# Optimization experiments

Hardware: AMD Instinct MI355X
Metric: run time of the kernel (lower is better)

Reference implementation:

```python
import jax, jax.numpy as jnp
import numpy as np
import math

B, S, E, H = 2, 2048, 1024, 16
D = E // H
EPS = 1e-5


def setup_inputs() -> dict:
    key = jax.random.key(0)
    ks = jax.random.split(key, 6)
    s = 1.0 / math.sqrt(E)
    return {
        "query": jax.random.normal(ks[0], (B, S, E), jnp.float32),
        "Wq": jax.random.normal(ks[1], (E, E), jnp.float32) * s,
        "bq": jnp.zeros((E,), jnp.float32),
        "Wk": jax.random.normal(ks[2], (E, E), jnp.float32) * s,
        "bk": jnp.zeros((E,), jnp.float32),
        "Wv": jax.random.normal(ks[3], (E, E), jnp.float32) * s,
        "bv": jnp.zeros((E,), jnp.float32),
        "Wo": jax.random.normal(ks[4], (E, E), jnp.float32) * s,
        "bo": jnp.zeros((E,), jnp.float32),
        "alpha": jnp.ones((1,), jnp.float32),
    }


def reference(query, Wq, bq, Wk, bk, Wv, bv, Wo, bo, alpha):
    # Q/K/V projections (nn.Linear: x @ W.T + b)
    q = (query @ Wq.T + bq).reshape(B, S, H, D)
    k = (query @ Wk.T + bk).reshape(B, S, H, D)
    v = (query @ Wv.T + bv).reshape(B, S, H, D)

    # YAT scores: (q.k)^2 / (||q-k||^2 + eps)
    qk = jnp.einsum('bqhd,bkhd->bhqk', q, k)          # [B,H,S,S]
    sq = jnp.einsum('bqhd,bqhd->bhq', q, q)           # ||q||^2
    sk = jnp.einsum('bkhd,bkhd->bhk', k, k)           # ||k||^2
    dist_sq = sq[..., :, None] + sk[..., None, :] - 2.0 * qk
    scores = (qk * qk) / (dist_sq + EPS)

    # learnable alpha scaling: scores * (sqrt(d)/log(1+d))^alpha
    scale = (jnp.sqrt(jnp.float32(D)) / jnp.log1p(jnp.float32(D))) ** alpha[0]
    scores = scores * scale

    attn = jax.nn.softmax(scores, axis=-1)
    out = jnp.einsum('bhqk,bkhd->bqhd', attn, v).reshape(B, S, E)
    return out @ Wo.T + bo
```

## Files before the change

kernel.cpp:

```cpp
#include <hip/hip_runtime.h>
#include <hip/hip_fp16.h>
#include <math.h>

#define BB 2
#define SS 2048
#define EE 1024
#define HH 16
#define DD 64
#define YAT_EPS 1e-5f
#define RR (BB * HH * SS)

typedef __attribute__((ext_vector_type(8))) short bf16x8;
typedef __attribute__((ext_vector_type(4))) short short4v;
typedef __attribute__((ext_vector_type(4))) float f32x4;
#define MFMA16(a, b, c) __builtin_amdgcn_mfma_f32_16x16x32_bf16((a), (b), (c), 0, 0, 0)

#if __has_builtin(__builtin_amdgcn_exp2f)
#define EXP2(x) __builtin_amdgcn_exp2f(x)
#else
#define EXP2(x) exp2f(x)
#endif
#if __has_builtin(__builtin_amdgcn_rcpf)
#define RCPF(x) __builtin_amdgcn_rcpf(x)
#else
#define RCPF(x) (1.0f / (x))
#endif

__device__ __forceinline__ unsigned short f2bf(float x) {
    unsigned int u = __float_as_uint(x);
    u += 0x7FFFu + ((u >> 16) & 1u);
    return (unsigned short)(u >> 16);
}
__device__ __forceinline__ float bf2f(unsigned short h) {
    return __uint_as_float(((unsigned int)h) << 16);
}
__device__ __forceinline__ short f2bf_t(float x) {
    return (short)(__float_as_uint(x) >> 16);
}

__device__ __forceinline__ void async_ld16(void* lds, const void* g) {
    __builtin_amdgcn_global_load_lds(
        (const __attribute__((address_space(1))) unsigned int*)g,
        (__attribute__((address_space(3))) unsigned int*)lds, 16, 0, 0);
}

__global__ __launch_bounds__(256) void split_f32(const float* __restrict__ in,
                                                 unsigned short* __restrict__ hi,
                                                 unsigned short* __restrict__ lo,
                                                 int n4) {
    int i = blockIdx.x * 256 + threadIdx.x;
    if (i >= n4) return;
    float4 v = ((const float4*)in)[i];
    ushort4 h, l;
    h.x = f2bf(v.x); l.x = f2bf(v.x - bf2f(h.x));
    h.y = f2bf(v.y); l.y = f2bf(v.y - bf2f(h.y));
    h.z = f2bf(v.z); l.z = f2bf(v.z - bf2f(h.z));
    h.w = f2bf(v.w); l.w = f2bf(v.w - bf2f(h.w));
    ((ushort4*)hi)[i] = h;
    ((ushort4*)lo)[i] = l;
}

__global__ __launch_bounds__(256) void split_w4(
        const float* __restrict__ Wq, const float* __restrict__ Wk,
        const float* __restrict__ Wv, const float* __restrict__ Wo,
        unsigned short* __restrict__ Whi, unsigned short* __restrict__ Wlo,
        unsigned short* __restrict__ Wohi) {
    int i = blockIdx.x * 256 + threadIdx.x;
    int y = blockIdx.y;
    const float* src = y == 0 ? Wq : y == 1 ? Wk : y == 2 ? Wv : Wo;
    unsigned short* hi = y < 3 ? Whi + (size_t)y * EE * EE : Wohi;
    float4 v = ((const float4*)src)[i];
    ushort4 h;
    h.x = f2bf(v.x); h.y = f2bf(v.y); h.z = f2bf(v.z); h.w = f2bf(v.w);
    ((ushort4*)hi)[i] = h;
    if (y < 2) {
        unsigned short* lo = Wlo + (size_t)y * EE * EE;
        ushort4 l;
        l.x = f2bf(v.x - bf2f(h.x));
        l.y = f2bf(v.y - bf2f(h.y));
        l.z = f2bf(v.z - bf2f(h.z));
        l.w = f2bf(v.w - bf2f(h.w));
        ((ushort4*)lo)[i] = l;
    }
}

template <int MODE, int PASSES>
__global__ __launch_bounds__(256, 2) void gemm3p(
        const unsigned short* __restrict__ Ahi, const unsigned short* __restrict__ Alo,
        const unsigned short* __restrict__ Bhi, const unsigned short* __restrict__ Blo,
        const float* __restrict__ bq, const float* __restrict__ bk,
        const float* __restrict__ bv,
        float* __restrict__ Cf,
        unsigned short* __restrict__ qhi, unsigned short* __restrict__ qlo,
        unsigned short* __restrict__ khi,
        unsigned short* __restrict__ v_sd,
        float* __restrict__ sqn, float* __restrict__ skn,
        int M, int N, int K) {
    __shared__ __align__(16) unsigned short LA_hi[128 * 32];
    __shared__ __align__(16) unsigned short LA_lo[128 * 32];
    __shared__ __align__(16) unsigned short LB_hi[128 * 32];
    __shared__ __align__(16) unsigned short LB_lo[128 * 32];

    const int t = threadIdx.x;
    const int w = t >> 6, lane = t & 63;
    const int quad = lane >> 4, lr = lane & 15;
    const int wy = w & 1, wx = w >> 1;
    const int m0 = blockIdx.y * 128, n0 = blockIdx.x * 128;

    const unsigned short* gsrc = nullptr;
    unsigned short* ldst = nullptr;
    if (w == 0)      { gsrc = Ahi + (size_t)m0 * K; ldst = LA_hi; }
    else if (w == 2) { gsrc = Bhi + (size_t)n0 * K; ldst = LB_hi; }
    else if (PASSES == 3 && w == 1) { gsrc = Alo + (size_t)m0 * K; ldst = LA_lo; }
    else if (PASSES == 3 && w == 3) { gsrc = Blo + (size_t)n0 * K; ldst = LB_lo; }
    const unsigned short* gl = gsrc ? gsrc + (size_t)(lane >> 2) * K + (lane & 3) * 8
                                    : nullptr;

    f32x4 acc[4][4];
    #pragma unroll
    for (int i = 0; i < 4; ++i)
        #pragma unroll
        for (int j = 0; j < 4; ++j)
            acc[i][j] = (f32x4){0.f, 0.f, 0.f, 0.f};

    for (int k0 = 0; k0 < K; k0 += 32) {
        __syncthreads();
        if (gl) {
            #pragma unroll
            for (int i = 0; i < 8; ++i)
                async_ld16(ldst + i * 512, gl + (size_t)i * 16 * K + k0);
        }
        __syncthreads();
        bf16x8 ah[4], al[4], bh_[4], bl_[4];
        #pragma unroll
        for (int i = 0; i < 4; ++i) {
            ah[i]  = *(const bf16x8*)&LA_hi[(wy * 64 + i * 16 + lr) * 32 + quad * 8];
            bh_[i] = *(const bf16x8*)&LB_hi[(wx * 64 + i * 16 + lr) * 32 + quad * 8];
            if (PASSES == 3) {
                al[i]  = *(const bf16x8*)&LA_lo[(wy * 64 + i * 16 + lr) * 32 + quad * 8];
                bl_[i] = *(const bf16x8*)&LB_lo[(wx * 64 + i * 16 + lr) * 32 + quad * 8];
            }
        }
        #pragma unroll
        for (int mg = 0; mg < 4; ++mg)
            #pragma unroll
            for (int ns = 0; ns < 4; ++ns) {
                f32x4 a = acc[mg][ns];
                a = MFMA16(ah[mg], bh_[ns], a);
                if (PASSES == 3) {
                    a = MFMA16(ah[mg], bl_[ns], a);
                    a = MFMA16(al[mg], bh_[ns], a);
                }
                acc[mg][ns] = a;
            }
    }

    const int ng = n0 + wx * 64;
    if (MODE == 0) {
        float bias_v[4];
        #pragma unroll
        for (int ns = 0; ns < 4; ++ns) bias_v[ns] = bq[ng + ns * 16 + lr];
        #pragma unroll
        for (int mg = 0; mg < 4; ++mg)
            #pragma unroll
            for (int r = 0; r < 4; ++r) {
                int m = m0 + wy * 64 + mg * 16 + quad * 4 + r;
                #pragma unroll
                for (int ns = 0; ns < 4; ++ns)
                    Cf[(size_t)m * N + ng + ns * 16 + lr] = acc[mg][ns][r] + bias_v[ns];
            }
    } else {
        const int path = MODE == 1 ? (ng >> 10) : 2;
        const int c = MODE == 1 ? (ng & 1023) : ng;
        const int h = c >> 6;
        const float* bias = path == 0 ? bq : path == 1 ? bk : bv;
        unsigned short* hi_p = path == 0 ? qhi : path == 1 ? khi : v_sd;
        float* nrm = path == 0 ? sqn : skn;
        float bias_v[4];
        #pragma unroll
        for (int ns = 0; ns < 4; ++ns) bias_v[ns] = bias[c + ns * 16 + lr];
        #pragma unroll
        for (int mg = 0; mg < 4; ++mg)
            #pragma unroll
            for (int r = 0; r < 4; ++r) {
                int m = m0 + wy * 64 + mg * 16 + quad * 4 + r;
                int b = m >> 11, s = m & (SS - 1);
                size_t base = ((size_t)(b * HH + h) * SS + s) * DD;
                float v4[4];
                #pragma unroll
                for (int ns = 0; ns < 4; ++ns) v4[ns] = acc[mg][ns][r] + bias_v[ns];
                if (path < 2) {
                    float pn = v4[0] * v4[0] + v4[1] * v4[1] + v4[2] * v4[2] + v4[3] * v4[3];
                    #pragma unroll
                    for (int off = 1; off < 16; off <<= 1) pn += __shfl_xor(pn, off);
                    if (lr == 0) nrm[(size_t)(b * HH + h) * SS + s] = pn;
                    #pragma unroll
                    for (int ns = 0; ns < 4; ++ns) {
                        unsigned short hv = f2bf(v4[ns]);
                        hi_p[base + ns * 16 + lr] = hv;
                        if (path == 0)
                            qlo[base + ns * 16 + lr] = f2bf(v4[ns] - bf2f(hv));
                    }
                } else {
                    #pragma unroll
                    for (int ns = 0; ns < 4; ++ns)
                        hi_p[base + ns * 16 + lr] = f2bf(v4[ns]);
                }
            }
    }
}

__global__ __launch_bounds__(256) void transpose_v(const unsigned short* __restrict__ v_sd,
                                                   unsigned short* __restrict__ vt) {
    __shared__ unsigned short T[64][65];
    const int t = threadIdx.x;
    const int bh = blockIdx.y, s0 = blockIdx.x * 64;
    {
        int sl = t >> 2, d4 = (t & 3) * 16;
        const unsigned short* src = &v_sd[((size_t)bh * SS + s0 + sl) * DD + d4];
        bf16x8 a = *(const bf16x8*)src;
        bf16x8 b = *(const bf16x8*)(src + 8);
        #pragma unroll
        for (int j = 0; j < 8; ++j) {
            T[sl][d4 + j] = (unsigned short)a[j];
            T[sl][d4 + 8 + j] = (unsigned short)b[j];
        }
    }
    __syncthreads();
    {
        int dl = t >> 2, s4 = (t & 3) * 16;
        bf16x8 a, b;
        #pragma unroll
        for (int j = 0; j < 8; ++j) {
            a[j] = (short)T[s4 + j][dl];
            b[j] = (short)T[s4 + 8 + j][dl];
        }
        unsigned short* dst = &vt[((size_t)bh * DD + dl) * SS + s0 + s4];
        *(bf16x8*)dst = a;
        *(bf16x8*)(dst + 8) = b;
    }
}

__global__ __launch_bounds__(256, 4) void yat_attn_mfma(
        const unsigned short* __restrict__ qhi, const unsigned short* __restrict__ qlo,
        const unsigned short* __restrict__ khi,
        const unsigned short* __restrict__ vt,
        const float* __restrict__ sqn, const float* __restrict__ skn,
        const float* __restrict__ alphap,
        __half* __restrict__ Opart, float2* __restrict__ mlpart) {
    __shared__ __align__(16) unsigned short Ks[2][4096];
    __shared__ __align__(16) unsigned short Ps[4][16 * 68];

    const int t = threadIdx.x;
    const int w = t >> 6, lane = t & 63;
    const int quad = lane >> 4, lr = lane & 15;
    const int qt = blockIdx.x, bh = blockIdx.y, z = blockIdx.z;
    const int row0 = qt * 64 + w * 16;
    const float cscale = powf(sqrtf((float)DD) / log1pf((float)DD), alphap[0])
                         * 1.4426950408889634f;

    bf16x8 qh[2], ql[2];
    #pragma unroll
    for (int kd = 0; kd < 2; ++kd) {
        size_t o = ((size_t)bh * SS + row0 + lr) * DD + kd * 32 + quad * 8;
        qh[kd] = *(const bf16x8*)&qhi[o];
        ql[kd] = *(const bf16x8*)&qlo[o];
    }
    const float sqe = sqn[(size_t)bh * SS + row0 + lr] + YAT_EPS;

    const int lrow = lane >> 3;
    const int lofs = lrow * 64 + (((lane & 7) ^ (lrow & 7)) << 3);
    const int sw = lr & 7;

    float m_r = -INFINITY, l_r = 0.f;
    f32x4 O[4];
    #pragma unroll
    for (int nd = 0; nd < 4; ++nd) O[nd] = (f32x4){0.f, 0.f, 0.f, 0.f};

    const int t0 = z * 16;
    const size_t khi_base = (size_t)bh * SS * 64 + (size_t)w * 16 * 64 + lofs;
    const size_t skn_base = (size_t)bh * SS + quad * 4;
    unsigned short* myP = Ps[w];

    #pragma unroll
    for (int i2 = 0; i2 < 2; ++i2)
        async_ld16(&Ks[0][w * 1024 + i2 * 512],
                   khi + khi_base + (size_t)t0 * 4096 + i2 * 512);

    for (int it = 0; it < 16; ++it) {
        const int p = it & 1;
        __syncthreads();
        if (it + 1 < 16) {
            #pragma unroll
            for (int i2 = 0; i2 < 2; ++i2)
                async_ld16(&Ks[p ^ 1][w * 1024 + i2 * 512],
                           khi + khi_base + (size_t)(t0 + it + 1) * 4096 + i2 * 512);
        }
        const int kbase = (t0 + it) * 64;
        const unsigned short* kb = Ks[p];
        f32x4 acc[4];
        f32x4 sk4[4];
        #pragma unroll
        for (int st = 0; st < 4; ++st) {
            const int rbase = (st * 16 + lr) * 64;
            bf16x8 kh0 = *(const bf16x8*)&kb[rbase + ((quad    ) ^ sw) * 8];
            bf16x8 kh1 = *(const bf16x8*)&kb[rbase + ((quad + 4) ^ sw) * 8];
            sk4[st] = *(const f32x4*)&skn[skn_base + kbase + st * 16];
            f32x4 a = (f32x4){0.f, 0.f, 0.f, 0.f};
            a = MFMA16(kh0, qh[0], a);
            a = MFMA16(kh1, qh[1], a);
            a = MFMA16(kh0, ql[0], a);
            a = MFMA16(kh1, ql[1], a);
            acc[st] = a;
        }
        bf16x8 vf[4][2];
        #pragma unroll
        for (int nd = 0; nd < 4; ++nd)
            #pragma unroll
            for (int kk = 0; kk < 2; ++kk)
                vf[nd][kk] = *(const bf16x8*)&vt[((size_t)bh * DD + nd * 16 + lr) * SS
                                                 + kbase + kk * 32 + quad * 8];
        float mx = -INFINITY;
        #pragma unroll
        for (int st = 0; st < 4; ++st)
            #pragma unroll
            for (int r = 0; r < 4; ++r) {
                float qk = acc[st][r];
                float d = sqe + sk4[st][r] - 2.f * qk;
                float u = qk * qk * RCPF(d);
                acc[st][r] = u;
                mx = fmaxf(mx, u);
            }
        mx = fmaxf(mx, __shfl_xor(mx, 16));
        mx = fmaxf(mx, __shfl_xor(mx, 32));
        float mnew = fmaxf(m_r, mx);
        bool resc = !__all(cscale * (mnew - m_r) <= 8.f);
        float aa = 1.f;
        if (resc) {
            aa = EXP2(__builtin_fmaf(cscale, m_r, -cscale * mnew));
            m_r = mnew;
        }
        const float cm = cscale * m_r;
        float rs = 0.f;
        #pragma unroll
        for (int st = 0; st < 4; ++st) {
            float e0 = EXP2(__builtin_fmaf(cscale, acc[st][0], -cm));
            float e1 = EXP2(__builtin_fmaf(cscale, acc[st][1], -cm));
            float e2 = EXP2(__builtin_fmaf(cscale, acc[st][2], -cm));
            float e3 = EXP2(__builtin_fmaf(cscale, acc[st][3], -cm));
            rs += (e0 + e1) + (e2 + e3);
            short4v pv;
            pv[0] = f2bf_t(e0); pv[1] = f2bf_t(e1);
            pv[2] = f2bf_t(e2); pv[3] = f2bf_t(e3);
            *(short4v*)&myP[lr * 68 + st * 16 + quad * 4] = pv;
        }
        rs += __shfl_xor(rs, 16);
        rs += __shfl_xor(rs, 32);
        l_r = l_r * aa + rs;
        if (resc) {
            float al_[4];
            #pragma unroll
            for (int r = 0; r < 4; ++r) al_[r] = __shfl(aa, quad * 4 + r);
            #pragma unroll
            for (int nd = 0; nd < 4; ++nd)
                #pragma unroll
                for (int r = 0; r < 4; ++r)
                    O[nd][r] *= al_[r];
        }
        bf16x8 pf[2];
        #pragma unroll
        for (int kk = 0; kk < 2; ++kk)
            pf[kk] = *(const bf16x8*)&myP[lr * 68 + kk * 32 + quad * 8];
        #pragma unroll
        for (int nd = 0; nd < 4; ++nd)
            #pragma unroll
            for (int kk = 0; kk < 2; ++kk)
                O[nd] = MFMA16(pf[kk], vf[nd][kk], O[nd]);
    }
    if (quad == 0)
        mlpart[(size_t)z * RR + (size_t)bh * SS + row0 + lr] =
            make_float2(cscale * m_r, l_r);
    #pragma unroll
    for (int r = 0; r < 4; ++r) {
        size_t rowg = (size_t)bh * SS + row0 + quad * 4 + r;
        #pragma unroll
        for (int nd = 0; nd < 4; ++nd)
            Opart[((size_t)z * RR + rowg) * DD + nd * 16 + lr] =
                __float2half(O[nd][r]);
    }
}

__global__ __launch_bounds__(256) void combine_attn(
        const __half* __restrict__ Opart, const float2* __restrict__ mlpart,
        unsigned short* __restrict__ ctxhi) {
    int tid = blockIdx.x * 256 + threadIdx.x;
    int row = tid >> 4, c4 = (tid & 15) * 4;
    float2 ml0 = mlpart[row];
    float2 ml1 = mlpart[RR + row];
    float ms = fmaxf(ml0.x, ml1.x);
    float a0 = EXP2(ml0.x - ms), a1 = EXP2(ml1.x - ms);
    float inv = RCPF(ml0.y * a0 + ml1.y * a1);
    a0 *= inv; a1 *= inv;
    const __half* p0 = Opart + (size_t)row * DD + c4;
    const __half* p1 = p0 + (size_t)RR * DD;
    int bh = row >> 11, s = row & (SS - 1);
    int b = bh >> 4, h = bh & 15;
    size_t idx = ((size_t)b * SS + s) * EE + h * DD + c4;
    ushort4 hv;
    unsigned short* hp = (unsigned short*)&hv;
    #pragma unroll
    for (int j = 0; j < 4; ++j) {
        float o = __half2float(p0[j]) * a0 + __half2float(p1[j]) * a1;
        hp[j] = f2bf(o);
    }
    *(ushort4*)&ctxhi[idx] = hv;
}

extern "C" void kernel_launch(void* const* d_in, const int* in_sizes, int n_in,
                              void* d_out, int out_size, void* d_ws, size_t ws_size,
                              hipStream_t stream) {
    const float* x     = (const float*)d_in[0];
    const float* Wq    = (const float*)d_in[1];
    const float* bq    = (const float*)d_in[2];
    const float* Wk    = (const float*)d_in[3];
    const float* bk    = (const float*)d_in[4];
    const float* Wv    = (const float*)d_in[5];
    const float* bv    = (const float*)d_in[6];
    const float* Wo    = (const float*)d_in[7];
    const float* bo    = (const float*)d_in[8];
    const float* alpha = (const float*)d_in[9];
    float* out = (float*)d_out;
    char* ws = (char*)d_ws;

    const int M = BB * SS;
    const size_t MB = 1u << 20;
    unsigned short* xhi  = (unsigned short*)(ws + 0 * MB);
    unsigned short* xlo  = (unsigned short*)(ws + 8 * MB);
    unsigned short* Whi  = (unsigned short*)(ws + 16 * MB);
    unsigned short* Wlo  = (unsigned short*)(ws + 22 * MB);
    unsigned short* vt   = (unsigned short*)(ws + 16 * MB);
    float2* mlpart       = (float2*)(ws + 24 * MB);
    unsigned short* Wohi = (unsigned short*)(ws + 28 * MB);
    unsigned short* qhi  = (unsigned short*)(ws + 32 * MB);
    unsigned short* qlo  = (unsigned short*)(ws + 40 * MB);
    unsigned short* khi  = (unsigned short*)(ws + 48 * MB);
    unsigned short* v_sd = (unsigned short*)(ws + 64 * MB);
    __half* Opart        = (__half*)(ws + 64 * MB);
    float* sqn = (float*)(ws + 80 * MB);
    float* skn = (float*)(ws + 80 * MB + 256 * 1024);
    unsigned short* ctxhi = xhi;

    const int nX = M * EE / 4, nW = EE * EE / 4;
    split_f32<<<nX / 256, 256, 0, stream>>>(x, xhi, xlo, nX);
    split_w4<<<dim3(nW / 256, 4), 256, 0, stream>>>(Wq, Wk, Wv, Wo, Whi, Wlo, Wohi);

    gemm3p<1, 3><<<dim3(2 * EE / 128, M / 128), 256, 0, stream>>>(
        xhi, xlo, Whi, Wlo, bq, bk, nullptr, nullptr,
        qhi, qlo, khi, nullptr, sqn, skn, M, 2 * EE, EE);
    gemm3p<2, 1><<<dim3(EE / 128, M / 128), 256, 0, stream>>>(
        xhi, nullptr, Whi + 2 * (size_t)EE * EE, nullptr, nullptr, nullptr, bv, nullptr,
        nullptr, nullptr, nullptr, v_sd, nullptr, nullptr, M, EE, EE);

    transpose_v<<<dim3(SS / 64, BB * HH), 256, 0, stream>>>(v_sd, vt);

    yat_attn_mfma<<<dim3(SS / 64, BB * HH, 2), 256, 0, stream>>>(
        qhi, qlo, khi, vt, sqn, skn, alpha, Opart, mlpart);

    combine_attn<<<RR * 16 / 256, 256, 0, stream>>>(Opart, mlpart, ctxhi);

    gemm3p<0, 1><<<dim3(EE / 128, M / 128), 256, 0, stream>>>(
        ctxhi, nullptr, Wohi, nullptr, bo, nullptr, nullptr, out,
        nullptr, nullptr, nullptr, nullptr, nullptr, nullptr, M, EE, EE);
}
```

Baseline: 358.2 us.

## Replace shared-memory K staging with register double-buffered direct global loads

Drops the LDS double buffer for K and the per-iteration __syncthreads. Each wave now loads its K fragments straight from global memory into registers, double-buffered across a manually unrolled pair of iterations. It also raises wave priority around the MFMA sections and lowers the occupancy hint from 4 to 3 blocks per CU to leave room for the extra registers. The aim is to remove barrier stalls and LDS traffic, at the cost of more register pressure and redundant global/L2 reads, since every wave now fetches the full K tile itself.

```diff
diff --git a/kernel.cpp b/kernel.cpp
--- a/kernel.cpp
+++ b/kernel.cpp
@@ -241,14 +241,121 @@
     }
 }
 
-__global__ __launch_bounds__(256, 4) void yat_attn_mfma(
+__device__ __forceinline__ void k_load(bf16x8 (&dst)[8],
+                                       const unsigned short* __restrict__ khi,
+                                       size_t krow, int tile, int lr, int quad) {
+    const unsigned short* kp = khi + (krow + (size_t)tile * 64) * DD;
+    dst[0] = *(const bf16x8*)&kp[(0 * 16 + lr) * 64      + quad * 8];
+    dst[1] = *(const bf16x8*)&kp[(0 * 16 + lr) * 64 + 32 + quad * 8];
+    dst[2] = *(const bf16x8*)&kp[(1 * 16 + lr) * 64      + quad * 8];
+    dst[3] = *(const bf16x8*)&kp[(1 * 16 + lr) * 64 + 32 + quad * 8];
+    dst[4] = *(const bf16x8*)&kp[(2 * 16 + lr) * 64      + quad * 8];
+    dst[5] = *(const bf16x8*)&kp[(2 * 16 + lr) * 64 + 32 + quad * 8];
+    dst[6] = *(const bf16x8*)&kp[(3 * 16 + lr) * 64      + quad * 8];
+    dst[7] = *(const bf16x8*)&kp[(3 * 16 + lr) * 64 + 32 + quad * 8];
+}
+
+__device__ __forceinline__ void yat_iter(
+        int itn, int t0,
+        const unsigned short* __restrict__ khi, size_t krow,
+        const unsigned short* __restrict__ vt, size_t vrow,
+        const float* __restrict__ skn, size_t skn_base,
+        const bf16x8 (&kcur)[8], bf16x8 (&knxt)[8],
+        const bf16x8 (&qh)[2], const bf16x8 (&ql)[2],
+        float sqe, float cscale,
+        unsigned short* myP, int lr, int quad,
+        float& m_r, float& l_r, f32x4 (&O)[4]) {
+    const int kbase = (t0 + itn) * 64;
+    if (itn + 1 < 16)
+        k_load(knxt, khi, krow, t0 + itn + 1, lr, quad);
+
+    f32x4 acc[4], sk4[4];
+    __builtin_amdgcn_s_setprio(1);
+    #pragma unroll
+    for (int st = 0; st < 4; ++st) {
+        sk4[st] = *(const f32x4*)&skn[skn_base + kbase + st * 16];
+        f32x4 a = (f32x4){0.f, 0.f, 0.f, 0.f};
+        a = MFMA16(kcur[st * 2], qh[0], a);
+        a = MFMA16(kcur[st * 2 + 1], qh[1], a);
+        a = MFMA16(kcur[st * 2], ql[0], a);
+        a = MFMA16(kcur[st * 2 + 1], ql[1], a);
+        acc[st] = a;
+    }
+    __builtin_amdgcn_s_setprio(0);
+    bf16x8 vf[4][2];
+    #pragma unroll
+    for (int nd = 0; nd < 4; ++nd)
+        #pragma unroll
+        for (int kk = 0; kk < 2; ++kk)
+            vf[nd][kk] = *(const bf16x8*)&vt[(vrow + nd * 16 + lr) * SS
+                                             + kbase + kk * 32 + quad * 8];
+    float mx = -INFINITY;
+    #pragma unroll
+    for (int st = 0; st < 4; ++st)
+        #pragma unroll
+        for (int r = 0; r < 4; ++r) {
+            float qk = acc[st][r];
+            float d = sqe + sk4[st][r] - 2.f * qk;
+            float u = qk * qk * RCPF(d);
+            acc[st][r] = u;
+            mx = fmaxf(mx, u);
+        }
+    mx = fmaxf(mx, __shfl_xor(mx, 16));
+    mx = fmaxf(mx, __shfl_xor(mx, 32));
+    float mnew = fmaxf(m_r, mx);
+    bool resc = !__all(cscale * (mnew - m_r) <= 8.f);
+    float aa = 1.f;
+    if (resc) {
+        aa = EXP2(__builtin_fmaf(cscale, m_r, -cscale * mnew));
+        m_r = mnew;
+    }
+    const float cm = cscale * m_r;
+    float rs = 0.f;
+    #pragma unroll
+    for (int st = 0; st < 4; ++st) {
+        float e0 = EXP2(__builtin_fmaf(cscale, acc[st][0], -cm));
+        float e1 = EXP2(__builtin_fmaf(cscale, acc[st][1], -cm));
+        float e2 = EXP2(__builtin_fmaf(cscale, acc[st][2], -cm));
+        float e3 = EXP2(__builtin_fmaf(cscale, acc[st][3], -cm));
+        rs += (e0 + e1) + (e2 + e3);
+        short4v pv;
+        pv[0] = f2bf_t(e0); pv[1] = f2bf_t(e1);
+        pv[2] = f2bf_t(e2); pv[3] = f2bf_t(e3);
+        *(short4v*)&myP[lr * 68 + st * 16 + quad * 4] = pv;
+    }
+    rs += __shfl_xor(rs, 16);
+    rs += __shfl_xor(rs, 32);
+    l_r = l_r * aa + rs;
+    if (resc) {
+        float al_[4];
+        #pragma unroll
+        for (int r = 0; r < 4; ++r) al_[r] = __shfl(aa, quad * 4 + r);
+        #pragma unroll
+        for (int nd = 0; nd < 4; ++nd)
+            #pragma unroll
+            for (int r = 0; r < 4; ++r)
+                O[nd][r] *= al_[r];
+    }
+    bf16x8 pf[2];
+    #pragma unroll
+    for (int kk = 0; kk < 2; ++kk)
+        pf[kk] = *(const bf16x8*)&myP[lr * 68 + kk * 32 + quad * 8];
+    __builtin_amdgcn_s_setprio(1);
+    #pragma unroll
+    for (int nd = 0; nd < 4; ++nd)
+        #pragma unroll
+        for (int kk = 0; kk < 2; ++kk)
+            O[nd] = MFMA16(pf[kk], vf[nd][kk], O[nd]);
+    __builtin_amdgcn_s_setprio(0);
+}
+
+__global__ __launch_bounds__(256, 3) void yat_attn_mfma(
         const unsigned short* __restrict__ qhi, const unsigned short* __restrict__ qlo,
         const unsigned short* __restrict__ khi,
         const unsigned short* __restrict__ vt,
         const float* __restrict__ sqn, const float* __restrict__ skn,
         const float* __restrict__ alphap,
         __half* __restrict__ Opart, float2* __restrict__ mlpart) {
-    __shared__ __align__(16) unsigned short Ks[2][4096];
     __shared__ __align__(16) unsigned short Ps[4][16 * 68];
 
     const int t = threadIdx.x;
@@ -268,115 +375,27 @@
     }
     const float sqe = sqn[(size_t)bh * SS + row0 + lr] + YAT_EPS;
 
-    const int lrow = lane >> 3;
-    const int lofs = lrow * 64 + (((lane & 7) ^ (lrow & 7)) << 3);
-    const int sw = lr & 7;
-
     float m_r = -INFINITY, l_r = 0.f;
     f32x4 O[4];
     #pragma unroll
     for (int nd = 0; nd < 4; ++nd) O[nd] = (f32x4){0.f, 0.f, 0.f, 0.f};
 
     const int t0 = z * 16;
-    const size_t khi_base = (size_t)bh * SS * 64 + (size_t)w * 16 * 64 + lofs;
+    const size_t krow = (size_t)bh * SS;
+    const size_t vrow = (size_t)bh * DD;
     const size_t skn_base = (size_t)bh * SS + quad * 4;
     unsigned short* myP = Ps[w];
 
-    #pragma unroll
-    for (int i2 = 0; i2 < 2; ++i2)
-        async_ld16(&Ks[0][w * 1024 + i2 * 512],
-                   khi + khi_base + (size_t)t0 * 4096 + i2 * 512);
-
-    for (int it = 0; it < 16; ++it) {
-        const int p = it & 1;
-        __syncthreads();
-        if (it + 1 < 16) {
-            #pragma unroll
-            for (int i2 = 0; i2 < 2; ++i2)
-                async_ld16(&Ks[p ^ 1][w * 1024 + i2 * 512],
-                           khi + khi_base + (size_t)(t0 + it + 1) * 4096 + i2 * 512);
-        }
-        const int kbase = (t0 + it) * 64;
-        const unsigned short* kb = Ks[p];
-        f32x4 acc[4];
-        f32x4 sk4[4];
-        #pragma unroll
-        for (int st = 0; st < 4; ++st) {
-            const int rbase = (st * 16 + lr) * 64;
-            bf16x8 kh0 = *(const bf16x8*)&kb[rbase + ((quad    ) ^ sw) * 8];
-            bf16x8 kh1 = *(const bf16x8*)&kb[rbase + ((quad + 4) ^ sw) * 8];
-            sk4[st] = *(const f32x4*)&skn[skn_base + kbase + st * 16];
-            f32x4 a = (f32x4){0.f, 0.f, 0.f, 0.f};
-            a = MFMA16(kh0, qh[0], a);
-            a = MFMA16(kh1, qh[1], a);
-            a = MFMA16(kh0, ql[0], a);
-            a = MFMA16(kh1, ql[1], a);
-            acc[st] = a;
-        }
-        bf16x8 vf[4][2];
-        #pragma unroll
-        for (int nd = 0; nd < 4; ++nd)
-            #pragma unroll
-            for (int kk = 0; kk < 2; ++kk)
-                vf[nd][kk] = *(const bf16x8*)&vt[((size_t)bh * DD + nd * 16 + lr) * SS
-                                                 + kbase + kk * 32 + quad * 8];
-        float mx = -INFINITY;
-        #pragma unroll
-        for (int st = 0; st < 4; ++st)
-            #pragma unroll
-            for (int r = 0; r < 4; ++r) {
-                float qk = acc[st][r];
-                float d = sqe + sk4[st][r] - 2.f * qk;
-                float u = qk * qk * RCPF(d);
-                acc[st][r] = u;
-                mx = fmaxf(mx, u);
-            }
-        mx = fmaxf(mx, __shfl_xor(mx, 16));
-        mx = fmaxf(mx, __shfl_xor(mx, 32));
-        float mnew = fmaxf(m_r, mx);
-        bool resc = !__all(cscale * (mnew - m_r) <= 8.f);
-        float aa = 1.f;
-        if (resc) {
-            aa = EXP2(__builtin_fmaf(cscale, m_r, -cscale * mnew));
-            m_r = mnew;
-        }
-        const float cm = cscale * m_r;
-        float rs = 0.f;
-        #pragma unroll
-        for (int st = 0; st < 4; ++st) {
-            float e0 = EXP2(__builtin_fmaf(cscale, acc[st][0], -cm));
-            float e1 = EXP2(__builtin_fmaf(cscale, acc[st][1], -cm));
-            float e2 = EXP2(__builtin_fmaf(cscale, acc[st][2], -cm));
-            float e3 = EXP2(__builtin_fmaf(cscale, acc[st][3], -cm));
-            rs += (e0 + e1) + (e2 + e3);
-            short4v pv;
-            pv[0] = f2bf_t(e0); pv[1] = f2bf_t(e1);
-            pv[2] = f2bf_t(e2); pv[3] = f2bf_t(e3);
-            *(short4v*)&myP[lr * 68 + st * 16 + quad * 4] = pv;
-        }
-        rs += __shfl_xor(rs, 16);
-        rs += __shfl_xor(rs, 32);
-        l_r = l_r * aa + rs;
-        if (resc) {
-            float al_[4];
-            #pragma unroll
-            for (int r = 0; r < 4; ++r) al_[r] = __shfl(aa, quad * 4 + r);
-            #pragma unroll
-            for (int nd = 0; nd < 4; ++nd)
-                #pragma unroll
-                for (int r = 0; r < 4; ++r)
-                    O[nd][r] *= al_[r];
-        }
-        bf16x8 pf[2];
-        #pragma unroll
-        for (int kk = 0; kk < 2; ++kk)
-            pf[kk] = *(const bf16x8*)&myP[lr * 68 + kk * 32 + quad * 8];
-        #pragma unroll
-        for (int nd = 0; nd < 4; ++nd)
-            #pragma unroll
-            for (int kk = 0; kk < 2; ++kk)
-                O[nd] = MFMA16(pf[kk], vf[nd][kk], O[nd]);
-    }
+    bf16x8 kA[8], kB[8];
+    k_load(kA, khi, krow, t0, lr, quad);
+
+    for (int it2 = 0; it2 < 8; ++it2) {
+        yat_iter(2 * it2,     t0, khi, krow, vt, vrow, skn, skn_base,
+                 kA, kB, qh, ql, sqe, cscale, myP, lr, quad, m_r, l_r, O);
+        yat_iter(2 * it2 + 1, t0, khi, krow, vt, vrow, skn, skn_base,
+                 kB, kA, qh, ql, sqe, cscale, myP, lr, quad, m_r, l_r, O);
+    }
+
     if (quad == 0)
         mlpart[(size_t)z * RR + (size_t)bh * SS + row0 + lr] =
             make_float2(cscale * m_r, l_r);
```

New measurement: 494.3 us. +38.0%, slower.

## Give each wave private double-buffered K tiles and drop block-wide barriers

Applied to the files above, without the earlier changes.

Each wave now stages its own 32-key K tile into a private double buffer in LDS and waits only on its own vmcnt, so the per-iteration __syncthreads is gone. The key tile per iteration shrinks from 64 to 32 keys, with twice as many iterations, and the MFMA sections are wrapped in s_setprio raises. The intent is to remove block synchronisation stalls and let waves run out of step. The cost is that each wave now loads all of K itself, where before the tile was shared across the four waves, so the block issues four times the K traffic into LDS. The loop also runs more iterations, each with its own softmax-rescale overhead.

```diff
diff --git a/kernel.cpp b/kernel.cpp
--- a/kernel.cpp
+++ b/kernel.cpp
@@ -241,6 +241,109 @@
     }
 }
 
+__device__ __forceinline__ void k_stage(unsigned short* dst,
+                                        const unsigned short* src) {
+    #pragma unroll
+    for (int j = 0; j < 4; ++j)
+        async_ld16(dst + j * 512, src + (size_t)j * 512);
+}
+
+__device__ __forceinline__ void yat_iter32(
+        int itn, int nt, int t0,
+        const unsigned short* __restrict__ kb, unsigned short* __restrict__ kn,
+        const unsigned short* __restrict__ khi_l,
+        const unsigned short* __restrict__ vt, size_t vrow,
+        const float* __restrict__ skn, size_t skn_base,
+        const bf16x8 (&qh)[2], const bf16x8 (&ql)[2],
+        float sqe, float cscale, unsigned short* __restrict__ myP,
+        int lr, int quad, int sw,
+        float& m_r, float& l_r, f32x4 (&O)[4]) {
+    const int kbase = (t0 + itn) * 32;
+    asm volatile("s_waitcnt vmcnt(0)" ::: "memory");
+    bf16x8 kf[2][2];
+    #pragma unroll
+    for (int st = 0; st < 2; ++st) {
+        const int rbase = (st * 16 + lr) * 64;
+        kf[st][0] = *(const bf16x8*)&kb[rbase + ((quad    ) ^ sw) * 8];
+        kf[st][1] = *(const bf16x8*)&kb[rbase + ((quad + 4) ^ sw) * 8];
+    }
+    f32x4 sk2[2];
+    #pragma unroll
+    for (int st = 0; st < 2; ++st)
+        sk2[st] = *(const f32x4*)&skn[skn_base + kbase + st * 16];
+    bf16x8 vf[4];
+    #pragma unroll
+    for (int nd = 0; nd < 4; ++nd)
+        vf[nd] = *(const bf16x8*)&vt[(vrow + nd * 16 + lr) * SS + kbase + quad * 8];
+    if (itn + 1 < nt)
+        k_stage(kn, khi_l + (size_t)(t0 + itn + 1) * 32 * DD);
+    f32x4 acc[2];
+    __builtin_amdgcn_s_setprio(1);
+    #pragma unroll
+    for (int st = 0; st < 2; ++st) {
+        f32x4 a = (f32x4){0.f, 0.f, 0.f, 0.f};
+        a = MFMA16(kf[st][0], qh[0], a);
+        a = MFMA16(kf[st][1], qh[1], a);
+        a = MFMA16(kf[st][0], ql[0], a);
+        a = MFMA16(kf[st][1], ql[1], a);
+        acc[st] = a;
+    }
+    __builtin_amdgcn_s_setprio(0);
+    float mx = -INFINITY;
+    #pragma unroll
+    for (int st = 0; st < 2; ++st)
+        #pragma unroll
+        for (int r = 0; r < 4; ++r) {
+            float qk = acc[st][r];
+            float d = sqe + sk2[st][r] - 2.f * qk;
+            float u = qk * qk * RCPF(d);
+            acc[st][r] = u;
+            mx = fmaxf(mx, u);
+        }
+    mx = fmaxf(mx, __shfl_xor(mx, 16));
+    mx = fmaxf(mx, __shfl_xor(mx, 32));
+    float mnew = fmaxf(m_r, mx);
+    bool resc = !__all(cscale * (mnew - m_r) <= 8.f);
+    float aa = 1.f;
+    if (resc) {
+        aa = EXP2(__builtin_fmaf(cscale, m_r, -cscale * mnew));
+        m_r = mnew;
+    }
+    const float cm = cscale * m_r;
+    float rs = 0.f;
+    #pragma unroll
+    for (int st = 0; st < 2; ++st) {
+        float e0 = EXP2(__builtin_fmaf(cscale, acc[st][0], -cm));
+        float e1 = EXP2(__builtin_fmaf(cscale, acc[st][1], -cm));
+        float e2 = EXP2(__builtin_fmaf(cscale, acc[st][2], -cm));
+        float e3 = EXP2(__builtin_fmaf(cscale, acc[st][3], -cm));
+        rs += (e0 + e1) + (e2 + e3);
+        short4v pv;
+        pv[0] = f2bf_t(e0); pv[1] = f2bf_t(e1);
+        pv[2] = f2bf_t(e2); pv[3] = f2bf_t(e3);
+        *(short4v*)&myP[lr * 40 + st * 16 + quad * 4] = pv;
+    }
+    rs += __shfl_xor(rs, 16);
+    rs += __shfl_xor(rs, 32);
+    l_r = l_r * aa + rs;
+    if (resc) {
+        float al_[4];
+        #pragma unroll
+        for (int r = 0; r < 4; ++r) al_[r] = __shfl(aa, quad * 4 + r);
+        #pragma unroll
+        for (int nd = 0; nd < 4; ++nd)
+            #pragma unroll
+            for (int r = 0; r < 4; ++r)
+                O[nd][r] *= al_[r];
+    }
+    bf16x8 pf = *(const bf16x8*)&myP[lr * 40 + quad * 8];
+    __builtin_amdgcn_s_setprio(1);
+    #pragma unroll
+    for (int nd = 0; nd < 4; ++nd)
+        O[nd] = MFMA16(pf, vf[nd], O[nd]);
+    __builtin_amdgcn_s_setprio(0);
+}
+
 __global__ __launch_bounds__(256, 4) void yat_attn_mfma(
         const unsigned short* __restrict__ qhi, const unsigned short* __restrict__ qlo,
         const unsigned short* __restrict__ khi,
@@ -248,8 +351,8 @@
         const float* __restrict__ sqn, const float* __restrict__ skn,
         const float* __restrict__ alphap,
         __half* __restrict__ Opart, float2* __restrict__ mlpart) {
-    __shared__ __align__(16) unsigned short Ks[2][4096];
-    __shared__ __align__(16) unsigned short Ps[4][16 * 68];
+    __shared__ __align__(16) unsigned short Ks[4][2][2048];
+    __shared__ __align__(16) unsigned short Ps[4][16 * 40];
 
     const int t = threadIdx.x;
     const int w = t >> 6, lane = t & 63;
@@ -277,106 +380,23 @@
     #pragma unroll
     for (int nd = 0; nd < 4; ++nd) O[nd] = (f32x4){0.f, 0.f, 0.f, 0.f};
 
-    const int t0 = z * 16;
-    const size_t khi_base = (size_t)bh * SS * 64 + (size_t)w * 16 * 64 + lofs;
+    const int t0 = z * 32;
+    const unsigned short* khi_l = khi + (size_t)bh * SS * DD + lofs;
+    const size_t vrow = (size_t)bh * DD;
     const size_t skn_base = (size_t)bh * SS + quad * 4;
     unsigned short* myP = Ps[w];
-
-    #pragma unroll
-    for (int i2 = 0; i2 < 2; ++i2)
-        async_ld16(&Ks[0][w * 1024 + i2 * 512],
-                   khi + khi_base + (size_t)t0 * 4096 + i2 * 512);
-
-    for (int it = 0; it < 16; ++it) {
-        const int p = it & 1;
-        __syncthreads();
-        if (it + 1 < 16) {
-            #pragma unroll
-            for (int i2 = 0; i2 < 2; ++i2)
-                async_ld16(&Ks[p ^ 1][w * 1024 + i2 * 512],
-                           khi + khi_base + (size_t)(t0 + it + 1) * 4096 + i2 * 512);
-        }
-        const int kbase = (t0 + it) * 64;
-        const unsigned short* kb = Ks[p];
-        f32x4 acc[4];
-        f32x4 sk4[4];
-        #pragma unroll
-        for (int st = 0; st < 4; ++st) {
-            const int rbase = (st * 16 + lr) * 64;
-            bf16x8 kh0 = *(const bf16x8*)&kb[rbase + ((quad    ) ^ sw) * 8];
-            bf16x8 kh1 = *(const bf16x8*)&kb[rbase + ((quad + 4) ^ sw) * 8];
-            sk4[st] = *(const f32x4*)&skn[skn_base + kbase + st * 16];
-            f32x4 a = (f32x4){0.f, 0.f, 0.f, 0.f};
-            a = MFMA16(kh0, qh[0], a);
-            a = MFMA16(kh1, qh[1], a);
-            a = MFMA16(kh0, ql[0], a);
-            a = MFMA16(kh1, ql[1], a);
-            acc[st] = a;
-        }
-        bf16x8 vf[4][2];
-        #pragma unroll
-        for (int nd = 0; nd < 4; ++nd)
-            #pragma unroll
-            for (int kk = 0; kk < 2; ++kk)
-                vf[nd][kk] = *(const bf16x8*)&vt[((size_t)bh * DD + nd * 16 + lr) * SS
-                                                 + kbase + kk * 32 + quad * 8];
-        float mx = -INFINITY;
-        #pragma unroll
-        for (int st = 0; st < 4; ++st)
-            #pragma unroll
-            for (int r = 0; r < 4; ++r) {
-                float qk = acc[st][r];
-                float d = sqe + sk4[st][r] - 2.f * qk;
-                float u = qk * qk * RCPF(d);
-                acc[st][r] = u;
-                mx = fmaxf(mx, u);
-            }
-        mx = fmaxf(mx, __shfl_xor(mx, 16));
-        mx = fmaxf(mx, __shfl_xor(mx, 32));
-        float mnew = fmaxf(m_r, mx);
-        bool resc = !__all(cscale * (mnew - m_r) <= 8.f);
-        float aa = 1.f;
-        if (resc) {
-            aa = EXP2(__builtin_fmaf(cscale, m_r, -cscale * mnew));
-            m_r = mnew;
-        }
-        const float cm = cscale * m_r;
-        float rs = 0.f;
-        #pragma unroll
-        for (int st = 0; st < 4; ++st) {
-            float e0 = EXP2(__builtin_fmaf(cscale, acc[st][0], -cm));
-            float e1 = EXP2(__builtin_fmaf(cscale, acc[st][1], -cm));
-            float e2 = EXP2(__builtin_fmaf(cscale, acc[st][2], -cm));
-            float e3 = EXP2(__builtin_fmaf(cscale, acc[st][3], -cm));
-            rs += (e0 + e1) + (e2 + e3);
-            short4v pv;
-            pv[0] = f2bf_t(e0); pv[1] = f2bf_t(e1);
-            pv[2] = f2bf_t(e2); pv[3] = f2bf_t(e3);
-            *(short4v*)&myP[lr * 68 + st * 16 + quad * 4] = pv;
-        }
-        rs += __shfl_xor(rs, 16);
-        rs += __shfl_xor(rs, 32);
-        l_r = l_r * aa + rs;
-        if (resc) {
-            float al_[4];
-            #pragma unroll
-            for (int r = 0; r < 4; ++r) al_[r] = __shfl(aa, quad * 4 + r);
-            #pragma unroll
-            for (int nd = 0; nd < 4; ++nd)
-                #pragma unroll
-                for (int r = 0; r < 4; ++r)
-                    O[nd][r] *= al_[r];
-        }
-        bf16x8 pf[2];
-        #pragma unroll
-        for (int kk = 0; kk < 2; ++kk)
-            pf[kk] = *(const bf16x8*)&myP[lr * 68 + kk * 32 + quad * 8];
-        #pragma unroll
-        for (int nd = 0; nd < 4; ++nd)
-            #pragma unroll
-            for (int kk = 0; kk < 2; ++kk)
-                O[nd] = MFMA16(pf[kk], vf[nd][kk], O[nd]);
-    }
+    unsigned short* k0 = Ks[w][0];
+    unsigned short* k1 = Ks[w][1];
+
+    k_stage(k0, khi_l + (size_t)t0 * 32 * DD);
+
+    for (int it2 = 0; it2 < 16; ++it2) {
+        yat_iter32(2 * it2,     32, t0, k0, k1, khi_l, vt, vrow, skn, skn_base,
+                   qh, ql, sqe, cscale, myP, lr, quad, sw, m_r, l_r, O);
+        yat_iter32(2 * it2 + 1, 32, t0, k1, k0, khi_l, vt, vrow, skn, skn_base,
+                   qh, ql, sqe, cscale, myP, lr, quad, sw, m_r, l_r, O);
+    }
+
     if (quad == 0)
         mlpart[(size_t)z * RR + (size_t)bh * SS + row0 + lr] =
             make_float2(cscale * m_r, l_r);
```

Measured after the change: 371.8 us. +3.8%, slower.

## Fuse Q/K/V projections into one launch with in-kernel V transpose

Applied to the files above, without the earlier changes.

Merges the 3-pass Q/K GEMM, the single-pass V GEMM and the separate V transpose kernel into one proj_qkv launch. The first 16 column blocks run the 3-pass Q/K path and the remaining 8 run the single-pass V path, which transposes its tile through shared memory and writes vt directly. This removes two kernel launches and the v_sd round trip through global memory, and lets the V blocks fill the tail of the Q/K grid. In exchange the kernel uses a larger shared buffer and has divergent work per block (3 MFMA passes versus 1), which may unbalance scheduling.

```diff
diff --git a/kernel.cpp b/kernel.cpp
--- a/kernel.cpp
+++ b/kernel.cpp
@@ -84,35 +84,39 @@
     }
 }
 
-template <int MODE, int PASSES>
-__global__ __launch_bounds__(256, 2) void gemm3p(
+__global__ __launch_bounds__(256, 2) void proj_qkv(
         const unsigned short* __restrict__ Ahi, const unsigned short* __restrict__ Alo,
-        const unsigned short* __restrict__ Bhi, const unsigned short* __restrict__ Blo,
+        const unsigned short* __restrict__ Whi, const unsigned short* __restrict__ Wlo,
         const float* __restrict__ bq, const float* __restrict__ bk,
         const float* __restrict__ bv,
-        float* __restrict__ Cf,
         unsigned short* __restrict__ qhi, unsigned short* __restrict__ qlo,
-        unsigned short* __restrict__ khi,
-        unsigned short* __restrict__ v_sd,
-        float* __restrict__ sqn, float* __restrict__ skn,
-        int M, int N, int K) {
-    __shared__ __align__(16) unsigned short LA_hi[128 * 32];
-    __shared__ __align__(16) unsigned short LA_lo[128 * 32];
-    __shared__ __align__(16) unsigned short LB_hi[128 * 32];
-    __shared__ __align__(16) unsigned short LB_lo[128 * 32];
-
+        unsigned short* __restrict__ khi, unsigned short* __restrict__ vt,
+        float* __restrict__ sqn, float* __restrict__ skn) {
+    __shared__ __align__(16) unsigned short SH[128 * 136];
+    unsigned short* LA_hi = SH;
+    unsigned short* LA_lo = SH + 4096;
+    unsigned short* LB_hi = SH + 8192;
+    unsigned short* LB_lo = SH + 12288;
+
+    const int K = EE;
     const int t = threadIdx.x;
     const int w = t >> 6, lane = t & 63;
     const int quad = lane >> 4, lr = lane & 15;
     const int wy = w & 1, wx = w >> 1;
-    const int m0 = blockIdx.y * 128, n0 = blockIdx.x * 128;
+    const bool p3 = blockIdx.x < 16;
+    const int m0 = blockIdx.y * 128;
+    const int n0 = p3 ? blockIdx.x * 128 : 0;
+    const int c0 = p3 ? 0 : (blockIdx.x - 16) * 128;
 
     const unsigned short* gsrc = nullptr;
     unsigned short* ldst = nullptr;
     if (w == 0)      { gsrc = Ahi + (size_t)m0 * K; ldst = LA_hi; }
-    else if (w == 2) { gsrc = Bhi + (size_t)n0 * K; ldst = LB_hi; }
-    else if (PASSES == 3 && w == 1) { gsrc = Alo + (size_t)m0 * K; ldst = LA_lo; }
-    else if (PASSES == 3 && w == 3) { gsrc = Blo + (size_t)n0 * K; ldst = LB_lo; }
+    else if (w == 2) {
+        gsrc = p3 ? Whi + (size_t)n0 * K
+                  : Whi + (size_t)(2 * EE + c0) * K;
+        ldst = LB_hi;
+    } else if (p3 && w == 1) { gsrc = Alo + (size_t)m0 * K; ldst = LA_lo; }
+    else if (p3 && w == 3)   { gsrc = Wlo + (size_t)n0 * K; ldst = LB_lo; }
     const unsigned short* gl = gsrc ? gsrc + (size_t)(lane >> 2) * K + (lane & 3) * 8
                                     : nullptr;
 
@@ -136,7 +140,7 @@
         for (int i = 0; i < 4; ++i) {
             ah[i]  = *(const bf16x8*)&LA_hi[(wy * 64 + i * 16 + lr) * 32 + quad * 8];
             bh_[i] = *(const bf16x8*)&LB_hi[(wx * 64 + i * 16 + lr) * 32 + quad * 8];
-            if (PASSES == 3) {
+            if (p3) {
                 al[i]  = *(const bf16x8*)&LA_lo[(wy * 64 + i * 16 + lr) * 32 + quad * 8];
                 bl_[i] = *(const bf16x8*)&LB_lo[(wx * 64 + i * 16 + lr) * 32 + quad * 8];
             }
@@ -147,7 +151,7 @@
             for (int ns = 0; ns < 4; ++ns) {
                 f32x4 a = acc[mg][ns];
                 a = MFMA16(ah[mg], bh_[ns], a);
-                if (PASSES == 3) {
+                if (p3) {
                     a = MFMA16(ah[mg], bl_[ns], a);
                     a = MFMA16(al[mg], bh_[ns], a);
                 }
@@ -155,26 +159,13 @@
             }
     }
 
-    const int ng = n0 + wx * 64;
-    if (MODE == 0) {
-        float bias_v[4];
-        #pragma unroll
-        for (int ns = 0; ns < 4; ++ns) bias_v[ns] = bq[ng + ns * 16 + lr];
-        #pragma unroll
-        for (int mg = 0; mg < 4; ++mg)
-            #pragma unroll
-            for (int r = 0; r < 4; ++r) {
-                int m = m0 + wy * 64 + mg * 16 + quad * 4 + r;
-                #pragma unroll
-                for (int ns = 0; ns < 4; ++ns)
-                    Cf[(size_t)m * N + ng + ns * 16 + lr] = acc[mg][ns][r] + bias_v[ns];
-            }
-    } else {
-        const int path = MODE == 1 ? (ng >> 10) : 2;
-        const int c = MODE == 1 ? (ng & 1023) : ng;
+    if (p3) {
+        const int ng = n0 + wx * 64;
+        const int path = ng >> 10;
+        const int c = ng & 1023;
         const int h = c >> 6;
-        const float* bias = path == 0 ? bq : path == 1 ? bk : bv;
-        unsigned short* hi_p = path == 0 ? qhi : path == 1 ? khi : v_sd;
+        const float* bias = path == 0 ? bq : bk;
+        unsigned short* hi_p = path == 0 ? qhi : khi;
         float* nrm = path == 0 ? sqn : skn;
         float bias_v[4];
         #pragma unroll
@@ -189,56 +180,111 @@
                 float v4[4];
                 #pragma unroll
                 for (int ns = 0; ns < 4; ++ns) v4[ns] = acc[mg][ns][r] + bias_v[ns];
-                if (path < 2) {
-                    float pn = v4[0] * v4[0] + v4[1] * v4[1] + v4[2] * v4[2] + v4[3] * v4[3];
-                    #pragma unroll
-                    for (int off = 1; off < 16; off <<= 1) pn += __shfl_xor(pn, off);
-                    if (lr == 0) nrm[(size_t)(b * HH + h) * SS + s] = pn;
-                    #pragma unroll
-                    for (int ns = 0; ns < 4; ++ns) {
-                        unsigned short hv = f2bf(v4[ns]);
-                        hi_p[base + ns * 16 + lr] = hv;
-                        if (path == 0)
-                            qlo[base + ns * 16 + lr] = f2bf(v4[ns] - bf2f(hv));
-                    }
-                } else {
-                    #pragma unroll
-                    for (int ns = 0; ns < 4; ++ns)
-                        hi_p[base + ns * 16 + lr] = f2bf(v4[ns]);
+                float pn = v4[0] * v4[0] + v4[1] * v4[1] + v4[2] * v4[2] + v4[3] * v4[3];
+                #pragma unroll
+                for (int off = 1; off < 16; off <<= 1) pn += __shfl_xor(pn, off);
+                if (lr == 0) nrm[(size_t)(b * HH + h) * SS + s] = pn;
+                #pragma unroll
+                for (int ns = 0; ns < 4; ++ns) {
+                    unsigned short hv = f2bf(v4[ns]);
+                    hi_p[base + ns * 16 + lr] = hv;
+                    if (path == 0)
+                        qlo[base + ns * 16 + lr] = f2bf(v4[ns] - bf2f(hv));
                 }
             }
-    }
-}
-
-__global__ __launch_bounds__(256) void transpose_v(const unsigned short* __restrict__ v_sd,
-                                                   unsigned short* __restrict__ vt) {
-    __shared__ unsigned short T[64][65];
+    } else {
+        __syncthreads();
+        float bias_v[4];
+        #pragma unroll
+        for (int ns = 0; ns < 4; ++ns) bias_v[ns] = bv[c0 + wx * 64 + ns * 16 + lr];
+        #pragma unroll
+        for (int mg = 0; mg < 4; ++mg)
+            #pragma unroll
+            for (int r = 0; r < 4; ++r) {
+                int mloc = wy * 64 + mg * 16 + quad * 4 + r;
+                #pragma unroll
+                for (int ns = 0; ns < 4; ++ns) {
+                    int cloc = wx * 64 + ns * 16 + lr;
+                    SH[cloc * 136 + mloc] = f2bf(acc[mg][ns][r] + bias_v[ns]);
+                }
+            }
+        __syncthreads();
+        const int b = m0 >> 11, s0 = m0 & (SS - 1);
+        #pragma unroll
+        for (int jc = 0; jc < 8; ++jc) {
+            int cl = (t >> 4) + jc * 16;
+            int sl = (t & 15) * 8;
+            bf16x8 vv = *(const bf16x8*)&SH[cl * 136 + sl];
+            int c = c0 + cl, h = c >> 6, d = c & 63;
+            *(bf16x8*)&vt[((size_t)(b * HH + h) * DD + d) * SS + s0 + sl] = vv;
+        }
+    }
+}
+
+template <int MODE, int PASSES>
+__global__ __launch_bounds__(256, 2) void gemm3p(
+        const unsigned short* __restrict__ Ahi, const unsigned short* __restrict__ Alo,
+        const unsigned short* __restrict__ Bhi, const unsigned short* __restrict__ Blo,
+        const float* __restrict__ bq,
+        float* __restrict__ Cf,
+        int M, int N, int K) {
+    __shared__ __align__(16) unsigned short LA_hi[128 * 32];
+    __shared__ __align__(16) unsigned short LB_hi[128 * 32];
+
     const int t = threadIdx.x;
-    const int bh = blockIdx.y, s0 = blockIdx.x * 64;
-    {
-        int sl = t >> 2, d4 = (t & 3) * 16;
-        const unsigned short* src = &v_sd[((size_t)bh * SS + s0 + sl) * DD + d4];
-        bf16x8 a = *(const bf16x8*)src;
-        bf16x8 b = *(const bf16x8*)(src + 8);
-        #pragma unroll
-        for (int j = 0; j < 8; ++j) {
-            T[sl][d4 + j] = (unsigned short)a[j];
-            T[sl][d4 + 8 + j] = (unsigned short)b[j];
-        }
-    }
-    __syncthreads();
-    {
-        int dl = t >> 2, s4 = (t & 3) * 16;
-        bf16x8 a, b;
-        #pragma unroll
-        for (int j = 0; j < 8; ++j) {
-            a[j] = (short)T[s4 + j][dl];
-            b[j] = (short)T[s4 + 8 + j][dl];
-        }
-        unsigned short* dst = &vt[((size_t)bh * DD + dl) * SS + s0 + s4];
-        *(bf16x8*)dst = a;
-        *(bf16x8*)(dst + 8) = b;
-    }
+    const int w = t >> 6, lane = t & 63;
+    const int quad = lane >> 4, lr = lane & 15;
+    const int wy = w & 1, wx = w >> 1;
+    const int m0 = blockIdx.y * 128, n0 = blockIdx.x * 128;
+
+    const unsigned short* gsrc = nullptr;
+    unsigned short* ldst = nullptr;
+    if (w == 0)      { gsrc = Ahi + (size_t)m0 * K; ldst = LA_hi; }
+    else if (w == 2) { gsrc = Bhi + (size_t)n0 * K; ldst = LB_hi; }
+    const unsigned short* gl = gsrc ? gsrc + (size_t)(lane >> 2) * K + (lane & 3) * 8
+                                    : nullptr;
+
+    f32x4 acc[4][4];
+    #pragma unroll
+    for (int i = 0; i < 4; ++i)
+        #pragma unroll
+        for (int j = 0; j < 4; ++j)
+            acc[i][j] = (f32x4){0.f, 0.f, 0.f, 0.f};
+
+    for (int k0 = 0; k0 < K; k0 += 32) {
+        __syncthreads();
+        if (gl) {
+            #pragma unroll
+            for (int i = 0; i < 8; ++i)
+                async_ld16(ldst + i * 512, gl + (size_t)i * 16 * K + k0);
+        }
+        __syncthreads();
+        bf16x8 ah[4], bh_[4];
+        #pragma unroll
+        for (int i = 0; i < 4; ++i) {
+            ah[i]  = *(const bf16x8*)&LA_hi[(wy * 64 + i * 16 + lr) * 32 + quad * 8];
+            bh_[i] = *(const bf16x8*)&LB_hi[(wx * 64 + i * 16 + lr) * 32 + quad * 8];
+        }
+        #pragma unroll
+        for (int mg = 0; mg < 4; ++mg)
+            #pragma unroll
+            for (int ns = 0; ns < 4; ++ns)
+                acc[mg][ns] = MFMA16(ah[mg], bh_[ns], acc[mg][ns]);
+    }
+
+    const int ng = n0 + wx * 64;
+    float bias_v[4];
+    #pragma unroll
+    for (int ns = 0; ns < 4; ++ns) bias_v[ns] = bq[ng + ns * 16 + lr];
+    #pragma unroll
+    for (int mg = 0; mg < 4; ++mg)
+        #pragma unroll
+        for (int r = 0; r < 4; ++r) {
+            int m = m0 + wy * 64 + mg * 16 + quad * 4 + r;
+            #pragma unroll
+            for (int ns = 0; ns < 4; ++ns)
+                Cf[(size_t)m * N + ng + ns * 16 + lr] = acc[mg][ns][r] + bias_v[ns];
+        }
 }
 
 __global__ __launch_bounds__(256, 4) void yat_attn_mfma(
@@ -438,13 +484,12 @@
     unsigned short* xlo  = (unsigned short*)(ws + 8 * MB);
     unsigned short* Whi  = (unsigned short*)(ws + 16 * MB);
     unsigned short* Wlo  = (unsigned short*)(ws + 22 * MB);
-    unsigned short* vt   = (unsigned short*)(ws + 16 * MB);
     float2* mlpart       = (float2*)(ws + 24 * MB);
     unsigned short* Wohi = (unsigned short*)(ws + 28 * MB);
     unsigned short* qhi  = (unsigned short*)(ws + 32 * MB);
     unsigned short* qlo  = (unsigned short*)(ws + 40 * MB);
     unsigned short* khi  = (unsigned short*)(ws + 48 * MB);
-    unsigned short* v_sd = (unsigned short*)(ws + 64 * MB);
+    unsigned short* vt   = (unsigned short*)(ws + 56 * MB);
     __half* Opart        = (__half*)(ws + 64 * MB);
     float* sqn = (float*)(ws + 80 * MB);
     float* skn = (float*)(ws + 80 * MB + 256 * 1024);
@@ -454,14 +499,9 @@
     split_f32<<<nX / 256, 256, 0, stream>>>(x, xhi, xlo, nX);
     split_w4<<<dim3(nW / 256, 4), 256, 0, stream>>>(Wq, Wk, Wv, Wo, Whi, Wlo, Wohi);
 
-    gemm3p<1, 3><<<dim3(2 * EE / 128, M / 128), 256, 0, stream>>>(
-        xhi, xlo, Whi, Wlo, bq, bk, nullptr, nullptr,
-        qhi, qlo, khi, nullptr, sqn, skn, M, 2 * EE, EE);
-    gemm3p<2, 1><<<dim3(EE / 128, M / 128), 256, 0, stream>>>(
-        xhi, nullptr, Whi + 2 * (size_t)EE * EE, nullptr, nullptr, nullptr, bv, nullptr,
-        nullptr, nullptr, nullptr, v_sd, nullptr, nullptr, M, EE, EE);
-
-    transpose_v<<<dim3(SS / 64, BB * HH), 256, 0, stream>>>(v_sd, vt);
+    proj_qkv<<<dim3(24, M / 128), 256, 0, stream>>>(
+        xhi, xlo, Whi, Wlo, bq, bk, bv,
+        qhi, qlo, khi, vt, sqn, skn);
 
     yat_attn_mfma<<<dim3(SS / 64, BB * HH, 2), 256, 0, stream>>>(
         qhi, qlo, khi, vt, sqn, skn, alpha, Opart, mlpart);
@@ -469,6 +509,5 @@
     combine_attn<<<RR * 16 / 256, 256, 0, stream>>>(Opart, mlpart, ctxhi);
 
     gemm3p<0, 1><<<dim3(EE / 128, M / 128), 256, 0, stream>>>(
-        ctxhi, nullptr, Wohi, nullptr, bo, nullptr, nullptr, out,
-        nullptr, nullptr, nullptr, nullptr, nullptr, nullptr, M, EE, EE);
-}
+        ctxhi, nullptr, Wohi, nullptr, bo, out, M, EE, EE);
+}
```

New measurement: 329.3 us. 8.1% less time.
